# Optimization experiments

Measured on AMD Instinct MI355X. Metric: run time of the kernel, lower is better.

## Reference

```python
import jax, jax.numpy as jnp
import numpy as np

K = 7          # neighbor volumes
PS = 7         # patch size (unfold.ps)
C = 3          # image channels -> F = C*PS*PS = 147
H = 256
W = 256
PAD = PS // 2
HP, WP = H + 2 * PAD, W + 2 * PAD


def _unfold(img, qindex):
    # img: [Ch, H, W]; extract PS x PS patches centered at each query pixel.
    # returns [Ch, Q, PS, PS]
    padded = jnp.pad(img, ((0, 0), (PAD, PAD), (PAD, PAD)))
    i = qindex // W
    j = qindex % W
    d = jnp.arange(PS)
    rows = i[:, None, None] + d[None, :, None]   # [Q,PS,1] in padded coords
    cols = j[:, None, None] + d[None, None, :]   # [Q,1,PS]
    return padded[:, rows, cols]                 # [Ch,Q,PS,PS]


def _fold(patches, qindex):
    # patches: [Q, Ch, PS, PS]; scatter-add centered patches into image canvas.
    Ch = patches.shape[1]
    i = qindex // W
    j = qindex % W
    d = jnp.arange(PS)
    rows = i[:, None, None] + d[None, :, None]
    cols = j[:, None, None] + d[None, None, :]
    flat = (rows * WP + cols).reshape(-1)                         # [Q*PS*PS]
    vals = patches.transpose(0, 2, 3, 1).reshape(-1, Ch)          # [Q*PS*PS, Ch]
    canvas = jnp.zeros((HP * WP, Ch), patches.dtype).at[flat].add(vals)
    canvas = canvas.reshape(HP, WP, Ch).transpose(2, 0, 1)
    return canvas[:, PAD:PAD + H, PAD:PAD + W]                    # [Ch,H,W]


def _nnn(D, log_temp, k):
    # Neural nearest neighbors (N3Net): D [Q,O] = -squared dists, log_temp [Q,1]
    logits = D / jnp.exp(log_temp)
    ws = []
    for _ in range(k):
        w = jax.nn.softmax(logits, axis=-1)
        ws.append(w)
        logits = logits + jnp.log(jnp.clip(1.0 - w, 1e-6))
    return jnp.stack(ws, axis=-1)  # [Q,O,k]


def setup_inputs() -> dict:
    key = jax.random.key(0)
    k1, k2, k3, k4, k5 = jax.random.split(key, 5)
    Q = H * W
    N = Q
    O = 32
    E = 64
    F = C * PS * PS
    return {
        "x": jax.random.normal(k1, (N, F), jnp.float32),
        "xe": jax.random.normal(k2, (N, E), jnp.float32),
        "ye": jax.random.normal(k3, (Q, E), jnp.float32),
        "log_temp": jax.random.normal(k4, (1, 1, H, W), jnp.float32),
        "cand_inds": jax.random.randint(k5, (Q, O), 0, N, jnp.int32),
        "qindex": jnp.arange(Q, dtype=jnp.int32),
    }


def reference(x, xe, ye, log_temp, cand_inds, qindex):
    Q, O = cand_inds.shape
    # --- search: L2^2 distances to O candidate database items per query ---
    xg = xe[cand_inds]                                            # [Q,O,E]
    d2 = (jnp.sum(ye * ye, -1, keepdims=True)
          + jnp.sum(xg * xg, -1)
          - 2.0 * jnp.einsum('qe,qoe->qo', ye, xg))               # [Q,O]
    dists = -d2
    # --- per-query log temperature: unfold + avgpool over the patch ---
    lt = _unfold(log_temp[0], qindex)                             # [1,Q,PS,PS]
    lt = lt.reshape(Q, PS * PS, 1).mean(axis=1)                   # [Q,1] (avgpool)
    # --- neural nearest neighbors weights ---
    Wmat = _nnn(dists, lt, K)                                     # [Q,O,K]
    # --- wpsum: weighted patch sum for each of the K neighbor volumes ---
    xp = x[cand_inds]                                             # [Q,O,F]
    z = jnp.einsum('qof,qok->kqf', xp, Wmat)                      # [K,Q,F]
    # rearrange 'k q (c ph pw) -> q (k c) ph pw'
    z = z.reshape(K, Q, C, PS, PS).transpose(1, 0, 2, 3, 4).reshape(Q, K * C, PS, PS)
    # --- fold aggregated patches and the weight counts back to image ---
    vid = _fold(z, qindex)                                        # [K*C,H,W]
    wvid = _fold(jnp.ones_like(z), qindex)                        # [K*C,H,W]
    return vid, wvid
```

## Files before the change

kernel.cpp:

```cpp
#include <hip/hip_runtime.h>
#include <math.h>

namespace {
constexpr int KNB  = 7;
constexpr int PS   = 7;
constexpr int CCH  = 3;
constexpr int IH   = 256;
constexpr int IW   = 256;
constexpr int PADR = 3;
constexpr int QN   = IH * IW;
constexpr int ON   = 32;
constexpr int EN   = 64;
constexpr int FN   = CCH * PS * PS;
constexpr int KC   = KNB * CCH;
constexpr int TQ   = 8;
constexpr int CH   = TQ + PS - 1;
constexpr int CELEM = KC * CH * CH;
}

__global__ __launch_bounds__(256) void n3_tile_kernel(
    const float* __restrict__ x,
    const float* __restrict__ xe,
    const float* __restrict__ ye,
    const float* __restrict__ log_temp,
    const int*   __restrict__ cand,
    const int*   __restrict__ qindex,
    float*       __restrict__ vid)
{
    __shared__ float canvas[CELEM];
    __shared__ float w_lds[4][ON][8];
    __shared__ int   c_lds[4][ON];

    const int wib  = threadIdx.x >> 6;
    const int lane = threadIdx.x & 63;
    const int by   = blockIdx.x / (IW / TQ);
    const int bx   = blockIdx.x - by * (IW / TQ);
    const int y0   = by * TQ;
    const int x0   = bx * TQ;

    for (int i = threadIdx.x; i < CELEM; i += 256) canvas[i] = 0.f;
    __syncthreads();

    for (int t = wib; t < TQ * TQ; t += 4) {
        const int ty = t >> 3;
        const int tx = t & 7;
        const int q  = (y0 + ty) * IW + (x0 + tx);

        const int qpix = qindex[q];
        const int qi = qpix / IW;
        const int qj = qpix - qi * IW;

        float ltv = 0.f;
        if (lane < PS * PS) {
            int pi = lane / PS, pj = lane % PS;
            int yy = qi + pi - PADR, xx = qj + pj - PADR;
            if (yy >= 0 && yy < IH && xx >= 0 && xx < IW)
                ltv = log_temp[yy * IW + xx];
        }
        #pragma unroll
        for (int s = 32; s >= 1; s >>= 1) ltv += __shfl_xor(ltv, s);
        const float itemp = expf(-ltv * (1.f / 49.f));

        float d2 = 0.f;
        if (lane < ON) {
            const int cidx = cand[q * ON + lane];
            c_lds[wib][lane] = cidx;
            const float4* xr = (const float4*)(xe + (size_t)cidx * EN);
            const float4* yr = (const float4*)(ye + (size_t)q * EN);
            float dot = 0.f, xn = 0.f, yn = 0.f;
            #pragma unroll
            for (int e = 0; e < EN / 4; ++e) {
                float4 a = xr[e];
                float4 b = yr[e];
                dot += a.x * b.x + a.y * b.y + a.z * b.z + a.w * b.w;
                xn  += a.x * a.x + a.y * a.y + a.z * a.z + a.w * a.w;
                yn  += b.x * b.x + b.y * b.y + b.z * b.z + b.w * b.w;
            }
            d2 = yn + xn - 2.f * dot;
        }

        float logit = -d2 * itemp;
        float wk[KNB];
        #pragma unroll
        for (int k = 0; k < KNB; ++k) {
            float m = logit;
            #pragma unroll
            for (int s = 16; s >= 1; s >>= 1) m = fmaxf(m, __shfl_xor(m, s));
            float ev = expf(logit - m);
            float ssum = ev;
            #pragma unroll
            for (int s = 16; s >= 1; s >>= 1) ssum += __shfl_xor(ssum, s);
            float w = ev / ssum;
            wk[k] = w;
            logit += logf(fmaxf(1.f - w, 1e-6f));
        }
        if (lane < ON) {
            #pragma unroll
            for (int k = 0; k < KNB; ++k) w_lds[wib][lane][k] = wk[k];
        }

        #pragma unroll
        for (int it = 0; it < 3; ++it) {
            const int f = it * 64 + lane;
            const bool act = f < FN;
            float acc[KNB];
            #pragma unroll
            for (int k = 0; k < KNB; ++k) acc[k] = 0.f;
            #pragma unroll 8
            for (int o = 0; o < ON; ++o) {
                const int cidx = c_lds[wib][o];
                const float xv = act ? x[(size_t)cidx * FN + f] : 0.f;
                #pragma unroll
                for (int k = 0; k < KNB; ++k) acc[k] += xv * w_lds[wib][o][k];
            }
            if (act) {
                const int c  = f / (PS * PS);
                const int r  = f - c * (PS * PS);
                const int pi = r / PS;
                const int pj = r - pi * PS;
                const int ly = qi + pi - y0;
                const int lx = qj + pj - x0;
                #pragma unroll
                for (int k = 0; k < KNB; ++k)
                    atomicAdd(&canvas[(k * CCH + c) * (CH * CH) + ly * CH + lx], acc[k]);
            }
        }
    }

    __syncthreads();

    for (int i = threadIdx.x; i < CELEM; i += 256) {
        const float v = canvas[i];
        if (v != 0.f) {
            const int ch  = i / (CH * CH);
            const int rem = i - ch * (CH * CH);
            const int ly  = rem / CH;
            const int lx  = rem - ly * CH;
            const int gy  = y0 - PADR + ly;
            const int gx  = x0 - PADR + lx;
            if (gy >= 0 && gy < IH && gx >= 0 && gx < IW)
                atomicAdd(&vid[(size_t)ch * QN + gy * IW + gx], v);
        }
    }
}

__global__ __launch_bounds__(256) void wvid_kernel(float* __restrict__ wvid) {
    int idx = blockIdx.x * blockDim.x + threadIdx.x;
    if (idx >= QN) return;
    int y  = idx / IW;
    int xx = idx - y * IW;
    int cy = min(PS - 1, y  + PADR) - max(0, y  - (IH - 1 - PADR)) + 1;
    int cx = min(PS - 1, xx + PADR) - max(0, xx - (IW - 1 - PADR)) + 1;
    float v = (float)(cy * cx);
    #pragma unroll
    for (int ch = 0; ch < KC; ++ch) wvid[(size_t)ch * QN + idx] = v;
}

extern "C" void kernel_launch(void* const* d_in, const int* in_sizes, int n_in,
                              void* d_out, int out_size, void* d_ws, size_t ws_size,
                              hipStream_t stream) {
    const float* x    = (const float*)d_in[0];
    const float* xe   = (const float*)d_in[1];
    const float* ye   = (const float*)d_in[2];
    const float* ltm  = (const float*)d_in[3];
    const int*   cand = (const int*)d_in[4];
    const int*   qidx = (const int*)d_in[5];

    float* vid  = (float*)d_out;
    float* wvid = vid + (size_t)KC * QN;

    hipMemsetAsync(vid, 0, (size_t)KC * QN * sizeof(float), stream);

    n3_tile_kernel<<<(IH / TQ) * (IW / TQ), 256, 0, stream>>>(x, xe, ye, ltm, cand, qidx, vid);
    wvid_kernel<<<(QN + 255) / 256, 256, 0, stream>>>(wvid);
}
```

Baseline: 611.4 us.

## Use 8 waves per tile and split embedding distance across both wave halves

Block size grows from 256 to 512 threads, so eight waves each own one tile column and walk its rows. The embedding distance computation now uses all 64 lanes, with each half-wave summing half of the 64-dim vectors and combining through a shuffle, where before only 32 lanes worked. Candidate indices are stored pre-multiplied by the feature stride to save address arithmetic in the gather loop. The larger block and the launch-bounds hint raise LDS and register pressure per block.

```diff
diff --git a/kernel.cpp b/kernel.cpp
--- a/kernel.cpp
+++ b/kernel.cpp
@@ -16,9 +16,10 @@
 constexpr int TQ   = 8;
 constexpr int CH   = TQ + PS - 1;
 constexpr int CELEM = KC * CH * CH;
+constexpr int NW   = 8;
 }
 
-__global__ __launch_bounds__(256) void n3_tile_kernel(
+__global__ __launch_bounds__(512, 8) void n3_tile_kernel(
     const float* __restrict__ x,
     const float* __restrict__ xe,
     const float* __restrict__ ye,
@@ -28,8 +29,8 @@
     float*       __restrict__ vid)
 {
     __shared__ float canvas[CELEM];
-    __shared__ float w_lds[4][ON][8];
-    __shared__ int   c_lds[4][ON];
+    __shared__ float w_lds[NW][ON][8];
+    __shared__ int   off_lds[NW][ON];
 
     const int wib  = threadIdx.x >> 6;
     const int lane = threadIdx.x & 63;
@@ -38,13 +39,11 @@
     const int y0   = by * TQ;
     const int x0   = bx * TQ;
 
-    for (int i = threadIdx.x; i < CELEM; i += 256) canvas[i] = 0.f;
+    for (int i = threadIdx.x; i < CELEM; i += 512) canvas[i] = 0.f;
     __syncthreads();
 
-    for (int t = wib; t < TQ * TQ; t += 4) {
-        const int ty = t >> 3;
-        const int tx = t & 7;
-        const int q  = (y0 + ty) * IW + (x0 + tx);
+    for (int ty = 0; ty < TQ; ++ty) {
+        const int q = (y0 + ty) * IW + (x0 + wib);
 
         const int qpix = qindex[q];
         const int qi = qpix / IW;
@@ -61,42 +60,43 @@
         for (int s = 32; s >= 1; s >>= 1) ltv += __shfl_xor(ltv, s);
         const float itemp = expf(-ltv * (1.f / 49.f));
 
-        float d2 = 0.f;
-        if (lane < ON) {
-            const int cidx = cand[q * ON + lane];
-            c_lds[wib][lane] = cidx;
-            const float4* xr = (const float4*)(xe + (size_t)cidx * EN);
-            const float4* yr = (const float4*)(ye + (size_t)q * EN);
+        const int o = lane & 31;
+        const int h = lane >> 5;
+        const int cidx = cand[q * ON + o];
+        if (lane < ON) off_lds[wib][o] = cidx * FN;
+        {
+            const float4* xr = (const float4*)(xe + (size_t)cidx * EN) + h * 8;
+            const float4* yr = (const float4*)(ye + (size_t)q * EN) + h * 8;
             float dot = 0.f, xn = 0.f, yn = 0.f;
             #pragma unroll
-            for (int e = 0; e < EN / 4; ++e) {
+            for (int e = 0; e < 8; ++e) {
                 float4 a = xr[e];
                 float4 b = yr[e];
                 dot += a.x * b.x + a.y * b.y + a.z * b.z + a.w * b.w;
                 xn  += a.x * a.x + a.y * a.y + a.z * a.z + a.w * a.w;
                 yn  += b.x * b.x + b.y * b.y + b.z * b.z + b.w * b.w;
             }
-            d2 = yn + xn - 2.f * dot;
-        }
-
-        float logit = -d2 * itemp;
-        float wk[KNB];
-        #pragma unroll
-        for (int k = 0; k < KNB; ++k) {
-            float m = logit;
+            float part = xn + yn - 2.f * dot;
+            part += __shfl_xor(part, 32);
+            float logit = -part * itemp;
+            float wk[KNB];
             #pragma unroll
-            for (int s = 16; s >= 1; s >>= 1) m = fmaxf(m, __shfl_xor(m, s));
-            float ev = expf(logit - m);
-            float ssum = ev;
-            #pragma unroll
-            for (int s = 16; s >= 1; s >>= 1) ssum += __shfl_xor(ssum, s);
-            float w = ev / ssum;
-            wk[k] = w;
-            logit += logf(fmaxf(1.f - w, 1e-6f));
-        }
-        if (lane < ON) {
-            #pragma unroll
-            for (int k = 0; k < KNB; ++k) w_lds[wib][lane][k] = wk[k];
+            for (int k = 0; k < KNB; ++k) {
+                float m = logit;
+                #pragma unroll
+                for (int s = 16; s >= 1; s >>= 1) m = fmaxf(m, __shfl_xor(m, s));
+                float ev = expf(logit - m);
+                float ssum = ev;
+                #pragma unroll
+                for (int s = 16; s >= 1; s >>= 1) ssum += __shfl_xor(ssum, s);
+                float w = ev / ssum;
+                wk[k] = w;
+                logit += logf(fmaxf(1.f - w, 1e-6f));
+            }
+            if (lane < ON) {
+                #pragma unroll
+                for (int k = 0; k < KNB; ++k) w_lds[wib][lane][k] = wk[k];
+            }
         }
 
         #pragma unroll
@@ -107,11 +107,11 @@
             #pragma unroll
             for (int k = 0; k < KNB; ++k) acc[k] = 0.f;
             #pragma unroll 8
-            for (int o = 0; o < ON; ++o) {
-                const int cidx = c_lds[wib][o];
-                const float xv = act ? x[(size_t)cidx * FN + f] : 0.f;
+            for (int oo = 0; oo < ON; ++oo) {
+                const int off = off_lds[wib][oo];
+                const float xv = act ? x[off + f] : 0.f;
                 #pragma unroll
-                for (int k = 0; k < KNB; ++k) acc[k] += xv * w_lds[wib][o][k];
+                for (int k = 0; k < KNB; ++k) acc[k] += xv * w_lds[wib][oo][k];
             }
             if (act) {
                 const int c  = f / (PS * PS);
@@ -129,7 +129,7 @@
 
     __syncthreads();
 
-    for (int i = threadIdx.x; i < CELEM; i += 256) {
+    for (int i = threadIdx.x; i < CELEM; i += 512) {
         const float v = canvas[i];
         if (v != 0.f) {
             const int ch  = i / (CH * CH);
@@ -171,6 +171,6 @@
 
     hipMemsetAsync(vid, 0, (size_t)KC * QN * sizeof(float), stream);
 
-    n3_tile_kernel<<<(IH / TQ) * (IW / TQ), 256, 0, stream>>>(x, xe, ye, ltm, cand, qidx, vid);
+    n3_tile_kernel<<<(IH / TQ) * (IW / TQ), 512, 0, stream>>>(x, xe, ye, ltm, cand, qidx, vid);
     wvid_kernel<<<(QN + 255) / 256, 256, 0, stream>>>(wvid);
 }
```

New measurement: 769.4 us. 1.26x slower.
